# Kernel tuning notes

Measured on AMD Instinct MI355X. Metric: run time of the kernel, lower is better.

The kernel has to match this reference:

```python
import jax, jax.numpy as jnp
import numpy as np

IMG = 1024.0          # image height == width
OUT = 7               # roi_size
RATIO = 2             # sampling_ratio
SCALE = 1.0 / 32.0    # spatial_scale
BBOX_W = (10.0, 10.0, 5.0, 5.0)
DWH_CLIP = float(np.log(1000.0 / 16.0))


def _bilinear(feat, ys, xs):
    """feat [C,H,W]; ys [N,P,1], xs [N,1,P] -> [C,N,P,P] (torchvision semantics)."""
    C, H, W = feat.shape
    valid = (ys > -1.0) & (ys < H) & (xs > -1.0) & (xs < W)
    y = jnp.clip(ys, 0.0, H - 1.0)
    x = jnp.clip(xs, 0.0, W - 1.0)
    y0 = jnp.floor(y).astype(jnp.int32)
    x0 = jnp.floor(x).astype(jnp.int32)
    y1 = jnp.minimum(y0 + 1, H - 1)
    x1 = jnp.minimum(x0 + 1, W - 1)
    ly = y - y0
    lx = x - x0
    hy = 1.0 - ly
    hx = 1.0 - lx
    v = (feat[:, y0, x0] * (hy * hx) + feat[:, y0, x1] * (hy * lx)
         + feat[:, y1, x0] * (ly * hx) + feat[:, y1, x1] * (ly * lx))
    return jnp.where(valid, v, 0.0)


def _roi_align_image(feat, rois):
    """feat [C,H,W], rois [N,4] xyxy in image coords -> [N,C,OUT,OUT]."""
    b = rois * SCALE
    x1, y1 = b[:, 0], b[:, 1]
    rw = jnp.maximum(b[:, 2] - x1, 1.0)
    rh = jnp.maximum(b[:, 3] - y1, 1.0)
    bw = rw / OUT
    bh = rh / OUT
    # sub-bin sample offsets: [OUT*RATIO] positions along each roi edge
    g = (jnp.arange(OUT, dtype=jnp.float32)[:, None]
         + (jnp.arange(RATIO, dtype=jnp.float32)[None, :] + 0.5) / RATIO).reshape(-1)
    ys = y1[:, None] + g[None, :] * bh[:, None]   # [N, OUT*RATIO]
    xs = x1[:, None] + g[None, :] * bw[:, None]
    v = _bilinear(feat, ys[:, :, None], xs[:, None, :])          # [C,N,P,P]
    C = feat.shape[0]
    v = v.reshape(C, -1, OUT, RATIO, OUT, RATIO).mean(axis=(3, 5))  # avg over samples
    return jnp.transpose(v, (1, 0, 2, 3))


def _decode(deltas, proposals):
    """deltas [R,K*4], proposals [R,4] -> clipped boxes [R,K,4]."""
    wx, wy, ww, wh = BBOX_W
    pw = proposals[:, 2] - proposals[:, 0]
    ph = proposals[:, 3] - proposals[:, 1]
    cx = proposals[:, 0] + 0.5 * pw
    cy = proposals[:, 1] + 0.5 * ph
    d = deltas.reshape(deltas.shape[0], -1, 4)
    dx = d[..., 0] / wx
    dy = d[..., 1] / wy
    dw = jnp.minimum(d[..., 2] / ww, DWH_CLIP)
    dh = jnp.minimum(d[..., 3] / wh, DWH_CLIP)
    pcx = dx * pw[:, None] + cx[:, None]
    pcy = dy * ph[:, None] + cy[:, None]
    ppw = jnp.exp(dw) * pw[:, None]
    pph = jnp.exp(dh) * ph[:, None]
    boxes = jnp.stack([pcx - 0.5 * ppw, pcy - 0.5 * pph,
                       pcx + 0.5 * ppw, pcy + 0.5 * pph], axis=-1)
    return jnp.clip(boxes, 0.0, IMG)  # clip_boxes_to_image


def setup_inputs() -> dict:
    key = jax.random.key(0)
    ks = jax.random.split(key, 8)
    B, N, C, H, W = 2, 1024, 256, 32, 32
    feat_dim = C * OUT * OUT  # 12544
    features = jax.random.normal(ks[0], (B, C, H, W), dtype=jnp.float32)
    cxy = jax.random.uniform(ks[1], (B, N, 2), minval=0.0, maxval=IMG)
    wh = jax.random.uniform(ks[2], (B, N, 2), minval=16.0, maxval=256.0)
    p1 = jnp.clip(cxy - 0.5 * wh, 0.0, IMG)
    p2 = jnp.clip(cxy + 0.5 * wh, 0.0, IMG)
    proposals = jnp.concatenate([p1, p2], axis=-1)  # [B,N,4] valid xyxy
    w1 = jax.random.normal(ks[3], (1024, feat_dim), dtype=jnp.float32) * 0.01
    w2 = jax.random.normal(ks[4], (1024, 1024), dtype=jnp.float32) * 0.01
    wc = jax.random.normal(ks[5], (2, 1024), dtype=jnp.float32) * 0.01
    wb = jax.random.normal(ks[6], (8, 1024), dtype=jnp.float32) * 0.001
    return {"features": features, "proposals": proposals,
            "w1": w1, "b1": jnp.zeros((1024,), jnp.float32),
            "w2": w2, "b2": jnp.zeros((1024,), jnp.float32),
            "wc": wc, "bc": jnp.zeros((2,), jnp.float32),
            "wb": wb, "bb": jnp.zeros((8,), jnp.float32)}


def reference(features, proposals, w1, b1, w2, b2, wc, bc, wb, bb):
    pooled = jax.vmap(_roi_align_image)(features, proposals)   # [B,N,C,7,7]
    B, N = pooled.shape[:2]
    x = pooled.reshape(B * N, -1)                               # flatten(start_dim=1)
    x = jax.nn.relu(x @ w1.T + b1)
    x = jax.nn.relu(x @ w2.T + b2)
    cls_scores = x @ wc.T + bc                                  # [R, num_classes]
    bbox_deltas = x @ wb.T + bb                                 # [R, num_classes*4]
    pred_boxes = _decode(bbox_deltas, proposals.reshape(-1, 4)) # [R, num_classes, 4]
    pred_scores = jax.nn.softmax(cls_scores, axis=-1)
    return cls_scores, bbox_deltas, pred_boxes, pred_scores
```

## Files before the change

kernel.cpp:

```cpp
#include <hip/hip_runtime.h>
#include <hip/hip_bf16.h>
#include <stdint.h>

typedef __attribute__((ext_vector_type(8))) short bf16x8;
typedef __attribute__((ext_vector_type(4))) float f32x4;

__device__ __forceinline__ ushort f2bf(float f) {
    union { float f; uint32_t u; } c; c.f = f;
    uint32_t u = c.u;
    uint32_t r = (u + 0x7FFFu + ((u >> 16) & 1u)) >> 16;
    return (ushort)r;
}

__device__ __forceinline__ void load16_to_lds(const void* gsrc, void* ldst) {
    __builtin_amdgcn_global_load_lds(
        (const __attribute__((address_space(1))) uint32_t*)gsrc,
        (__attribute__((address_space(3))) uint32_t*)ldst,
        16, 0, 0);
}

__global__ __launch_bounds__(256) void f32_to_bf16_kernel(
    const float* __restrict__ in, ushort* __restrict__ out, int n)
{
    int i = (blockIdx.x * 256 + threadIdx.x) * 4;
    if (i >= n) return;
    float4 v = *(const float4*)(in + i);
    ushort4 o;
    o.x = f2bf(v.x); o.y = f2bf(v.y); o.z = f2bf(v.z); o.w = f2bf(v.w);
    *(ushort4*)(out + i) = o;
}

__global__ __launch_bounds__(256) void transpose_feat_kernel(
    const float* __restrict__ feat, float* __restrict__ featT)
{
    int bc = blockIdx.x;
    int b = bc >> 8;
    int c = bc & 255;
    const float* src = feat + (size_t)bc * 1024;
    float* dst = featT + (size_t)b * 262144 + c;
    #pragma unroll
    for (int i = 0; i < 4; ++i) {
        int p = i * 256 + threadIdx.x;
        dst[(size_t)p * 256] = src[p];
    }
}

__global__ __launch_bounds__(512) void roi_align_kernel(
    const float* __restrict__ featT, const float* __restrict__ props,
    ushort* __restrict__ pooled)
{
    int roi = blockIdx.x;
    int b = roi >> 10;
    __shared__ int   si0[28];
    __shared__ int   si1[28];
    __shared__ float sl[28];
    __shared__ float sv[28];
    __shared__ float Aw[7][10];
    __shared__ float Bw[7][10];
    __shared__ __align__(16) ushort outbuf[12544];
    int tid = threadIdx.x;
    if (tid < 28) {
        int axis = (tid >= 14) ? 1 : 0;
        int pp = tid - axis * 14;
        float c0 = props[roi * 4 + (axis ? 0 : 1)] * (1.f / 32.f);
        float c1 = props[roi * 4 + (axis ? 2 : 3)] * (1.f / 32.f);
        float sz = fmaxf(c1 - c0, 1.f);
        float bsz = sz * (1.f / 7.f);
        float g = (float)(pp >> 1) + ((float)(pp & 1) + 0.5f) * 0.5f;
        float c = c0 + g * bsz;
        float valid = (c > -1.f && c < 32.f) ? 1.f : 0.f;
        float cc = fminf(fmaxf(c, 0.f), 31.f);
        float fl = floorf(cc);
        int i0 = (int)fl;
        si0[tid] = i0;
        si1[tid] = min(i0 + 1, 31);
        sl[tid] = cc - fl;
        sv[tid] = valid;
    }
    __syncthreads();

    const int r0 = si0[0];
    const int c0 = si0[14];

    if (tid < 140) {
        int axis = tid / 70;
        int e = tid - axis * 70;
        int oy = e / 10, yy = e - oy * 10;
        int base = axis * 14;
        int org = axis ? c0 : r0;
        float wsum = 0.f;
        #pragma unroll
        for (int s = 0; s < 2; ++s) {
            int p = base + oy * 2 + s;
            float w = 0.f;
            if (si0[p] - org == yy) w += 1.f - sl[p];
            if (si1[p] - org == yy) w += sl[p];
            wsum += sv[p] * w;
        }
        wsum *= 0.5f;
        if (axis == 0) Aw[oy][yy] = wsum;
        else           Bw[oy][yy] = wsum;
    }
    __syncthreads();

    const int grp = tid >> 8;
    const int ch = tid & 255;
    const float* fbase = featT + (size_t)b * 262144 + ch;

    int xoff[10];
    #pragma unroll
    for (int x = 0; x < 10; ++x) xoff[x] = min(c0 + x, 31) * 256;

    if (grp == 0) {
        float t[4][10];
        #pragma unroll
        for (int oy = 0; oy < 4; ++oy)
            #pragma unroll
            for (int x = 0; x < 10; ++x) t[oy][x] = 0.f;
        #pragma unroll
        for (int y = 0; y < 10; ++y) {
            const float* frow = fbase + (size_t)min(r0 + y, 31) * 8192;
            float a0 = Aw[0][y], a1 = Aw[1][y], a2 = Aw[2][y], a3 = Aw[3][y];
            #pragma unroll
            for (int x = 0; x < 10; ++x) {
                float fv = frow[xoff[x]];
                t[0][x] += a0 * fv;
                t[1][x] += a1 * fv;
                t[2][x] += a2 * fv;
                t[3][x] += a3 * fv;
            }
        }
        #pragma unroll
        for (int oy = 0; oy < 4; ++oy)
            #pragma unroll
            for (int ox = 0; ox < 7; ++ox) {
                float o = 0.f;
                #pragma unroll
                for (int x = 0; x < 10; ++x) o += Bw[ox][x] * t[oy][x];
                outbuf[ch * 49 + oy * 7 + ox] = f2bf(o);
            }
    } else {
        float t[3][10];
        #pragma unroll
        for (int oy = 0; oy < 3; ++oy)
            #pragma unroll
            for (int x = 0; x < 10; ++x) t[oy][x] = 0.f;
        #pragma unroll
        for (int y = 0; y < 10; ++y) {
            const float* frow = fbase + (size_t)min(r0 + y, 31) * 8192;
            float a4 = Aw[4][y], a5 = Aw[5][y], a6 = Aw[6][y];
            #pragma unroll
            for (int x = 0; x < 10; ++x) {
                float fv = frow[xoff[x]];
                t[0][x] += a4 * fv;
                t[1][x] += a5 * fv;
                t[2][x] += a6 * fv;
            }
        }
        #pragma unroll
        for (int oy = 0; oy < 3; ++oy)
            #pragma unroll
            for (int ox = 0; ox < 7; ++ox) {
                float o = 0.f;
                #pragma unroll
                for (int x = 0; x < 10; ++x) o += Bw[ox][x] * t[oy][x];
                outbuf[ch * 49 + (4 + oy) * 7 + ox] = f2bf(o);
            }
    }
    __syncthreads();

    const uint4* src = (const uint4*)outbuf;
    uint4* dst = (uint4*)(pooled + (size_t)roi * 12544);
    #pragma unroll
    for (int i = 0; i < 4; ++i) {
        int idx = i * 512 + tid;
        if (idx < 1568) dst[idx] = src[idx];
    }
}

__global__ __launch_bounds__(256) void gemm_bt_split(
    const ushort* __restrict__ A, const ushort* __restrict__ Bm,
    float* __restrict__ part, int M, int N, int K, int klen)
{
    constexpr int BK = 32;
    __shared__ __align__(16) ushort lA[2][128][BK];
    __shared__ __align__(16) ushort lB[2][128][BK];
    const int tid = threadIdx.x;

    const int nbx = gridDim.x, nby = gridDim.y;
    const int nwg = nbx * nby * gridDim.z;
    const int d = blockIdx.x + nbx * (blockIdx.y + nby * blockIdx.z);
    const int t = (d & 7) * (nwg >> 3) + (d >> 3);
    const int n_blk = t % nbx;
    const int m_blk = (t / nbx) % nby;
    const int k_blk = t / (nbx * nby);

    const int m0 = m_blk * 128;
    const int n0 = n_blk * 128;
    const int k_start = k_blk * klen;

    const int w = tid >> 6, l = tid & 63;
    const int wr = w >> 1, wcid = w & 1;
    const int lrow = l & 15;
    const int lkb = (((l >> 4) ^ ((lrow >> 1) & 3)) * 16);

    const int sc0 = tid, sc1 = 256 + tid;
    const int srow0 = sc0 >> 2, srow1 = sc1 >> 2;
    const int scol0 = ((sc0 & 3) ^ ((srow0 >> 1) & 3)) * 16;
    const int scol1 = ((sc1 & 3) ^ ((srow1 >> 1) & 3)) * 16;

    const int nsteps = klen / BK;

    {
        int k0 = k_start;
        load16_to_lds((const char*)(A + (size_t)(m0 + srow0) * K + k0) + scol0, ((char*)lA[0]) + sc0 * 16);
        load16_to_lds((const char*)(A + (size_t)(m0 + srow1) * K + k0) + scol1, ((char*)lA[0]) + sc1 * 16);
        load16_to_lds((const char*)(Bm + (size_t)(n0 + srow0) * K + k0) + scol0, ((char*)lB[0]) + sc0 * 16);
        load16_to_lds((const char*)(Bm + (size_t)(n0 + srow1) * K + k0) + scol1, ((char*)lB[0]) + sc1 * 16);
    }
    __syncthreads();

    f32x4 acc[4][4] = {};
    int cur = 0;

    for (int ts = 0; ts < nsteps; ++ts) {
        if (ts + 1 < nsteps) {
            int k0 = k_start + (ts + 1) * BK;
            int nxt = cur ^ 1;
            load16_to_lds((const char*)(A + (size_t)(m0 + srow0) * K + k0) + scol0, ((char*)lA[nxt]) + sc0 * 16);
            load16_to_lds((const char*)(A + (size_t)(m0 + srow1) * K + k0) + scol1, ((char*)lA[nxt]) + sc1 * 16);
            load16_to_lds((const char*)(Bm + (size_t)(n0 + srow0) * K + k0) + scol0, ((char*)lB[nxt]) + sc0 * 16);
            load16_to_lds((const char*)(Bm + (size_t)(n0 + srow1) * K + k0) + scol1, ((char*)lB[nxt]) + sc1 * 16);
        }

        bf16x8 af[4], bfr[4];
        #pragma unroll
        for (int m = 0; m < 4; ++m)
            af[m] = *(const bf16x8*)(((const char*)lA[cur]) + (wr * 64 + m * 16 + lrow) * 64 + lkb);
        #pragma unroll
        for (int n = 0; n < 4; ++n)
            bfr[n] = *(const bf16x8*)(((const char*)lB[cur]) + (wcid * 64 + n * 16 + lrow) * 64 + lkb);
        #pragma unroll
        for (int m = 0; m < 4; ++m)
            #pragma unroll
            for (int n = 0; n < 4; ++n)
                acc[m][n] = __builtin_amdgcn_mfma_f32_16x16x32_bf16(af[m], bfr[n], acc[m][n], 0, 0, 0);

        __syncthreads();
        cur ^= 1;
    }

    const int r4 = (l >> 4) * 4;
    const int cc = l & 15;
    float* pb = part + (size_t)k_blk * M * N;
    #pragma unroll
    for (int m = 0; m < 4; ++m) {
        #pragma unroll
        for (int n = 0; n < 4; ++n) {
            int col = n0 + wcid * 64 + n * 16 + cc;
            #pragma unroll
            for (int j = 0; j < 4; ++j) {
                int row = m0 + wr * 64 + m * 16 + r4 + j;
                pb[(size_t)row * N + col] = acc[m][n][j];
            }
        }
    }
}

template<bool OUT_BF16>
__global__ __launch_bounds__(256) void reduce_split_kernel(
    const float* __restrict__ part, const float* __restrict__ bias,
    void* __restrict__ out, int MN, int N, int S, int relu)
{
    int i4 = (blockIdx.x * 256 + threadIdx.x) * 4;
    if (i4 >= MN) return;
    float4 a = *(const float4*)(part + i4);
    for (int s = 1; s < S; ++s) {
        float4 b = *(const float4*)(part + (size_t)s * MN + i4);
        a.x += b.x; a.y += b.y; a.z += b.z; a.w += b.w;
    }
    int bc = i4 & (N - 1);
    float4 bv = *(const float4*)(bias + bc);
    a.x += bv.x; a.y += bv.y; a.z += bv.z; a.w += bv.w;
    if (relu) {
        a.x = fmaxf(a.x, 0.f); a.y = fmaxf(a.y, 0.f);
        a.z = fmaxf(a.z, 0.f); a.w = fmaxf(a.w, 0.f);
    }
    if (OUT_BF16) {
        ushort4 o; o.x = f2bf(a.x); o.y = f2bf(a.y); o.z = f2bf(a.z); o.w = f2bf(a.w);
        *(ushort4*)((ushort*)out + i4) = o;
    } else {
        *(float4*)((float*)out + i4) = a;
    }
}

template<bool OUT_BF16>
__global__ __launch_bounds__(256) void gemm_bt(
    const ushort* __restrict__ A, const ushort* __restrict__ Bm,
    const float* __restrict__ bias, void* __restrict__ Cout,
    int M, int N, int K, int relu)
{
    constexpr int BM = 128, BN = 64, BK = 32;
    __shared__ __align__(16) ushort lA[BM][BK];
    __shared__ __align__(16) ushort lB[BN][BK];
    const int tid = threadIdx.x;
    const int m0 = blockIdx.y * BM;
    const int n0 = blockIdx.x * BN;
    const int w = tid >> 6, l = tid & 63;
    const int wr = w >> 1, wcid = w & 1;
    const int lrow = l & 15, lk = (l >> 4) * 8;

    f32x4 acc[4][2] = {};

    for (int k0 = 0; k0 < K; k0 += BK) {
        __syncthreads();
        #pragma unroll
        for (int i = 0; i < 2; ++i) {
            int chunk = i * 256 + tid;
            int row = chunk >> 2;
            int colb = (chunk & 3) * 16;
            load16_to_lds((const char*)(A + (size_t)(m0 + row) * K + k0) + colb, ((char*)lA) + chunk * 16);
        }
        {
            int chunk = tid;
            int row = chunk >> 2;
            int colb = (chunk & 3) * 16;
            load16_to_lds((const char*)(Bm + (size_t)(n0 + row) * K + k0) + colb, ((char*)lB) + chunk * 16);
        }
        __syncthreads();

        bf16x8 af[4], bfr[2];
        #pragma unroll
        for (int m = 0; m < 4; ++m)
            af[m] = *(const bf16x8*)&lA[wr * 64 + m * 16 + lrow][lk];
        #pragma unroll
        for (int n = 0; n < 2; ++n)
            bfr[n] = *(const bf16x8*)&lB[wcid * 32 + n * 16 + lrow][lk];
        #pragma unroll
        for (int m = 0; m < 4; ++m)
            #pragma unroll
            for (int n = 0; n < 2; ++n)
                acc[m][n] = __builtin_amdgcn_mfma_f32_16x16x32_bf16(af[m], bfr[n], acc[m][n], 0, 0, 0);
    }

    const int r4 = (l >> 4) * 4;
    const int cc = l & 15;
    #pragma unroll
    for (int m = 0; m < 4; ++m) {
        #pragma unroll
        for (int n = 0; n < 2; ++n) {
            int col = n0 + wcid * 32 + n * 16 + cc;
            float bv = bias[col];
            #pragma unroll
            for (int j = 0; j < 4; ++j) {
                int row = m0 + wr * 64 + m * 16 + r4 + j;
                float v = acc[m][n][j] + bv;
                if (relu) v = fmaxf(v, 0.f);
                if (OUT_BF16) ((ushort*)Cout)[(size_t)row * N + col] = f2bf(v);
                else          ((float*)Cout)[(size_t)row * N + col] = v;
            }
        }
    }
}

__global__ __launch_bounds__(256) void heads_kernel(
    const float* __restrict__ x2,
    const float* __restrict__ wc, const float* __restrict__ bc,
    const float* __restrict__ wb, const float* __restrict__ bb,
    float* __restrict__ out)
{
    int w = threadIdx.x >> 6, l = threadIdx.x & 63;
    int row = blockIdx.x * 4 + w;
    const float* xr = x2 + (size_t)row * 1024;
    float acc[10];
    #pragma unroll
    for (int o = 0; o < 10; ++o) acc[o] = 0.f;
    for (int i = 0; i < 16; ++i) {
        int k = i * 64 + l;
        float xv = xr[k];
        #pragma unroll
        for (int o = 0; o < 2; ++o) acc[o] += xv * wc[o * 1024 + k];
        #pragma unroll
        for (int o = 0; o < 8; ++o) acc[2 + o] += xv * wb[o * 1024 + k];
    }
    #pragma unroll
    for (int o = 0; o < 10; ++o) {
        float v = acc[o];
        #pragma unroll
        for (int s = 32; s > 0; s >>= 1) v += __shfl_xor(v, s, 64);
        acc[o] = v;
    }
    if (l == 0) {
        float* cls = out;
        float* bbx = out + 2048 * 2;
        cls[row * 2 + 0] = acc[0] + bc[0];
        cls[row * 2 + 1] = acc[1] + bc[1];
        #pragma unroll
        for (int o = 0; o < 8; ++o) bbx[row * 8 + o] = acc[2 + o] + bb[o];
    }
}

__global__ __launch_bounds__(256) void decode_kernel(
    const float* __restrict__ props, float* __restrict__ out)
{
    int r = blockIdx.x * 256 + threadIdx.x;
    if (r >= 2048) return;
    const float* cls = out;
    const float* bbx = out + 4096;
    float* boxes  = out + 20480;
    float* scores = out + 36864;
    float px1 = props[r * 4 + 0], py1 = props[r * 4 + 1];
    float px2 = props[r * 4 + 2], py2 = props[r * 4 + 3];
    float pw = px2 - px1, ph = py2 - py1;
    float cx = px1 + 0.5f * pw, cy = py1 + 0.5f * ph;
    const float CLIP = 4.135166556742356f;
    #pragma unroll
    for (int k = 0; k < 2; ++k) {
        float dx = bbx[r * 8 + k * 4 + 0] * 0.1f;
        float dy = bbx[r * 8 + k * 4 + 1] * 0.1f;
        float dw = fminf(bbx[r * 8 + k * 4 + 2] * 0.2f, CLIP);
        float dh = fminf(bbx[r * 8 + k * 4 + 3] * 0.2f, CLIP);
        float pcx = dx * pw + cx, pcy = dy * ph + cy;
        float ppw = expf(dw) * pw, pph = expf(dh) * ph;
        float v0 = pcx - 0.5f * ppw, v1 = pcy - 0.5f * pph;
        float v2 = pcx + 0.5f * ppw, v3 = pcy + 0.5f * pph;
        boxes[r * 8 + k * 4 + 0] = fminf(fmaxf(v0, 0.f), 1024.f);
        boxes[r * 8 + k * 4 + 1] = fminf(fmaxf(v1, 0.f), 1024.f);
        boxes[r * 8 + k * 4 + 2] = fminf(fmaxf(v2, 0.f), 1024.f);
        boxes[r * 8 + k * 4 + 3] = fminf(fmaxf(v3, 0.f), 1024.f);
    }
    float s0 = cls[r * 2], s1 = cls[r * 2 + 1];
    float m = fmaxf(s0, s1);
    float e0 = expf(s0 - m), e1 = expf(s1 - m);
    float inv = 1.f / (e0 + e1);
    scores[r * 2 + 0] = e0 * inv;
    scores[r * 2 + 1] = e1 * inv;
}

extern "C" void kernel_launch(void* const* d_in, const int* in_sizes, int n_in,
                              void* d_out, int out_size, void* d_ws, size_t ws_size,
                              hipStream_t stream) {
    const float* feat  = (const float*)d_in[0];
    const float* props = (const float*)d_in[1];
    const float* w1    = (const float*)d_in[2];
    const float* b1    = (const float*)d_in[3];
    const float* w2    = (const float*)d_in[4];
    const float* b2    = (const float*)d_in[5];
    const float* wc    = (const float*)d_in[6];
    const float* bc    = (const float*)d_in[7];
    const float* wb    = (const float*)d_in[8];
    const float* bb    = (const float*)d_in[9];
    float* out = (float*)d_out;

    char* ws = (char*)d_ws;
    ushort* pooled = (ushort*)(ws);
    ushort* w1b    = (ushort*)(ws + 51380224);
    ushort* w2b    = (ushort*)(ws + 51380224 + 25690112);
    ushort* x1     = (ushort*)(ws + 79167488);
    float*  x2     = (float*) (ws + 83361792);
    float*  featT  = (float*) (ws + 83361792);
    float*  part   = (float*) (ws + 91750400);
    const size_t WS_NEED4 = 91750400 + 33554432;
    const size_t WS_NEED8 = 91750400 + 67108864;

    const int M = 2048, N = 1024;
    const int MN = M * N;

    f32_to_bf16_kernel<<<12845056 / 1024, 256, 0, stream>>>(w1, w1b, 12845056);
    f32_to_bf16_kernel<<<1048576 / 1024, 256, 0, stream>>>(w2, w2b, 1048576);
    transpose_feat_kernel<<<512, 256, 0, stream>>>(feat, featT);
    roi_align_kernel<<<2048, 512, 0, stream>>>(featT, props, pooled);

    if (ws_size >= WS_NEED8) {
        gemm_bt_split<<<dim3(N / 128, M / 128, 8), 256, 0, stream>>>(pooled, w1b, part, M, N, 12544, 1568);
        reduce_split_kernel<true ><<<MN / 1024, 256, 0, stream>>>(part, b1, x1, MN, N, 8, 1);
        gemm_bt_split<<<dim3(N / 128, M / 128, 4), 256, 0, stream>>>(x1, w2b, part, M, N, 1024, 256);
        reduce_split_kernel<false><<<MN / 1024, 256, 0, stream>>>(part, b2, x2, MN, N, 4, 1);
    } else if (ws_size >= WS_NEED4) {
        gemm_bt_split<<<dim3(N / 128, M / 128, 4), 256, 0, stream>>>(pooled, w1b, part, M, N, 12544, 3136);
        reduce_split_kernel<true ><<<MN / 1024, 256, 0, stream>>>(part, b1, x1, MN, N, 4, 1);
        gemm_bt_split<<<dim3(N / 128, M / 128, 4), 256, 0, stream>>>(x1, w2b, part, M, N, 1024, 256);
        reduce_split_kernel<false><<<MN / 1024, 256, 0, stream>>>(part, b2, x2, MN, N, 4, 1);
    } else {
        gemm_bt<true ><<<dim3(N / 64, M / 128), 256, 0, stream>>>(pooled, w1b, b1, x1, M, N, 12544, 1);
        gemm_bt<false><<<dim3(N / 64, M / 128), 256, 0, stream>>>(x1, w2b, b2, x2, M, N, 1024, 1);
    }

    heads_kernel<<<512, 256, 0, stream>>>(x2, wc, bc, wb, bb, out);
    decode_kernel<<<8, 256, 0, stream>>>(props, out);
}
```

Measured before the change: 185.6 us.

## Add 256x256 eight-wave pipelined GEMM for first FC layer with 7-way split-K

```diff
diff --git a/kernel.cpp b/kernel.cpp
--- a/kernel.cpp
+++ b/kernel.cpp
@@ -18,6 +18,10 @@
         (__attribute__((address_space(3))) uint32_t*)ldst,
         16, 0, 0);
 }
+
+#define FENCE() asm volatile("" ::: "memory")
+#define BARRIER() do { FENCE(); __builtin_amdgcn_s_barrier(); FENCE(); } while (0)
+#define VMCNT(n) asm volatile("s_waitcnt vmcnt(" #n ")" ::: "memory")
 
 __global__ __launch_bounds__(256) void f32_to_bf16_kernel(
     const float* __restrict__ in, ushort* __restrict__ out, int n)
@@ -178,6 +182,120 @@
     }
 }
 
+#define STAGE_A8(BB, HALF, KOFF) do { \
+    _Pragma("unroll") for (int r_ = 0; r_ < 2; ++r_) { \
+        int rbase_ = (HALF) * 128 + r_ * 64 + w * 8; \
+        int row_ = rbase_ + (l >> 3); \
+        int c16s_ = (l & 7) ^ (row_ & 7); \
+        load16_to_lds((const char*)(Ap + (size_t)(m0 + row_) * K + (KOFF)) + c16s_ * 16, \
+                      &sA[BB][rbase_][0]); \
+    } } while (0)
+#define STAGE_B8(BB, Q, KOFF) do { \
+    _Pragma("unroll") for (int r_ = 0; r_ < 2; ++r_) { \
+        int rl_ = r_ * 64 + w * 8 + (l >> 3); \
+        int brow_ = ((rl_ >> 5) << 6) + (Q) * 32 + (rl_ & 31); \
+        int c16s_ = (l & 7) ^ (rl_ & 7); \
+        load16_to_lds((const char*)(Bp + (size_t)(n0 + brow_) * K + (KOFF)) + c16s_ * 16, \
+                      &sB[BB][(Q) * 128 + r_ * 64 + w * 8][0]); \
+    } } while (0)
+#define PHASE8(QM, QN, STAGE_CODE, WAIT_CODE) do { \
+    STAGE_CODE; \
+    WAIT_CODE; \
+    BARRIER(); \
+    bf16x8 av_[8], bv_[4]; \
+    _Pragma("unroll") for (int mm_ = 0; mm_ < 4; ++mm_) \
+        _Pragma("unroll") for (int kk_ = 0; kk_ < 2; ++kk_) { \
+            int lr_ = wm * 128 + (QM) * 64 + mm_ * 16 + lrow; \
+            int c16s_ = (kk_ * 4 + khi) ^ (lrow & 7); \
+            av_[mm_ * 2 + kk_] = *(const bf16x8*)&sA[cur][lr_][c16s_ * 8]; \
+        } \
+    _Pragma("unroll") for (int nn_ = 0; nn_ < 2; ++nn_) \
+        _Pragma("unroll") for (int kk_ = 0; kk_ < 2; ++kk_) { \
+            int lrB_ = (QN) * 128 + wn * 32 + nn_ * 16 + lrow; \
+            int c16s_ = (kk_ * 4 + khi) ^ (lrow & 7); \
+            bv_[nn_ * 2 + kk_] = *(const bf16x8*)&sB[cur][lrB_][c16s_ * 8]; \
+        } \
+    __builtin_amdgcn_s_setprio(1); \
+    _Pragma("unroll") for (int mm_ = 0; mm_ < 4; ++mm_) \
+        _Pragma("unroll") for (int nn_ = 0; nn_ < 2; ++nn_) \
+            _Pragma("unroll") for (int kk_ = 0; kk_ < 2; ++kk_) \
+                acc[(QM) * 4 + mm_][(QN) * 2 + nn_] = __builtin_amdgcn_mfma_f32_16x16x32_bf16( \
+                    av_[mm_ * 2 + kk_], bv_[nn_ * 2 + kk_], acc[(QM) * 4 + mm_][(QN) * 2 + nn_], 0, 0, 0); \
+    __builtin_amdgcn_s_setprio(0); \
+    BARRIER(); \
+} while (0)
+
+__global__ __launch_bounds__(512) void gemm_8ph(
+    const ushort* __restrict__ Ap, const ushort* __restrict__ Bp,
+    float* __restrict__ part, int M, int N, int K, int klen)
+{
+    __shared__ __align__(16) ushort sA[2][256][64];
+    __shared__ __align__(16) ushort sB[2][256][64];
+    const int tid = threadIdx.x;
+
+    const int nbx = gridDim.x, nby = gridDim.y;
+    const int nwg = nbx * nby * gridDim.z;
+    const int d = blockIdx.x + nbx * (blockIdx.y + nby * blockIdx.z);
+    const int t = (d & 7) * (nwg >> 3) + (d >> 3);
+    const int n_blk = t % nbx;
+    const int m_blk = (t / nbx) % nby;
+    const int k_blk = t / (nbx * nby);
+
+    const int m0 = m_blk * 256;
+    const int n0 = n_blk * 256;
+    const int k_start = k_blk * klen;
+    const int nt = klen >> 6;
+
+    const int w = tid >> 6, l = tid & 63;
+    const int wm = w >> 2, wn = w & 3;
+    const int lrow = l & 15, khi = l >> 4;
+
+    f32x4 acc[8][4] = {};
+
+    {
+        int k0 = k_start, k1 = k_start + 64;
+        STAGE_B8(0, 0, k0);
+        STAGE_A8(0, 1, k0);
+        STAGE_A8(0, 0, k0);
+        STAGE_B8(0, 1, k0);
+        STAGE_B8(1, 0, k1);
+        STAGE_A8(1, 1, k1);
+    }
+
+    int cur = 0;
+    for (int T = 0; T < nt - 1; ++T) {
+        const int koff1 = k_start + (T + 1) * 64;
+        const int koff2 = k_start + (T + 2) * 64;
+        const int nxt = cur ^ 1;
+        const bool has2 = (T + 2) < nt;
+        PHASE8(0, 0, { STAGE_A8(nxt, 0, koff1); }, VMCNT(8));
+        PHASE8(1, 0, { STAGE_B8(nxt, 1, koff1); }, );
+        PHASE8(1, 1, { if (has2) STAGE_B8(cur, 0, koff2); }, VMCNT(8));
+        PHASE8(0, 1, { if (has2) STAGE_A8(cur, 1, koff2); }, );
+        cur ^= 1;
+    }
+    PHASE8(0, 0, , VMCNT(2));
+    PHASE8(1, 0, , );
+    PHASE8(1, 1, , VMCNT(0));
+    PHASE8(0, 1, , );
+
+    const int r4 = (l >> 4) * 4;
+    const int cc = l & 15;
+    float* pb = part + (size_t)k_blk * M * N;
+    #pragma unroll
+    for (int m = 0; m < 8; ++m) {
+        #pragma unroll
+        for (int n = 0; n < 4; ++n) {
+            int col = n0 + wn * 64 + n * 16 + cc;
+            #pragma unroll
+            for (int j = 0; j < 4; ++j) {
+                int row = m0 + wm * 128 + m * 16 + r4 + j;
+                pb[(size_t)row * N + col] = acc[m][n][j];
+            }
+        }
+    }
+}
+
 __global__ __launch_bounds__(256) void gemm_bt_split(
     const ushort* __restrict__ A, const ushort* __restrict__ Bm,
     float* __restrict__ part, int M, int N, int K, int klen)
@@ -460,8 +578,8 @@
     float*  x2     = (float*) (ws + 83361792);
     float*  featT  = (float*) (ws + 83361792);
     float*  part   = (float*) (ws + 91750400);
+    const size_t WS_NEED7 = 91750400 + (size_t)7 * 8388608;
     const size_t WS_NEED4 = 91750400 + 33554432;
-    const size_t WS_NEED8 = 91750400 + 67108864;
 
     const int M = 2048, N = 1024;
     const int MN = M * N;
@@ -471,9 +589,9 @@
     transpose_feat_kernel<<<512, 256, 0, stream>>>(feat, featT);
     roi_align_kernel<<<2048, 512, 0, stream>>>(featT, props, pooled);
 
-    if (ws_size >= WS_NEED8) {
-        gemm_bt_split<<<dim3(N / 128, M / 128, 8), 256, 0, stream>>>(pooled, w1b, part, M, N, 12544, 1568);
-        reduce_split_kernel<true ><<<MN / 1024, 256, 0, stream>>>(part, b1, x1, MN, N, 8, 1);
+    if (ws_size >= WS_NEED7) {
+        gemm_8ph<<<dim3(N / 256, M / 256, 7), 512, 0, stream>>>(pooled, w1b, part, M, N, 12544, 1792);
+        reduce_split_kernel<true ><<<MN / 1024, 256, 0, stream>>>(part, b1, x1, MN, N, 7, 1);
         gemm_bt_split<<<dim3(N / 128, M / 128, 4), 256, 0, stream>>>(x1, w2b, part, M, N, 1024, 256);
         reduce_split_kernel<false><<<MN / 1024, 256, 0, stream>>>(part, b2, x2, MN, N, 4, 1);
     } else if (ws_size >= WS_NEED4) {
```

After: 193.2 us. +4.1%, slower.
